# Kernel tuning notes

Measured on AMD Instinct MI355X. Metric: run time of the kernel, lower is better.

Reference implementation:

```python
import jax, jax.numpy as jnp
import numpy as np

N_NODES = 100000
N_EDGES = 1600000
HID = 128
HEADS = 8
DK = HID // HEADS
N_LAYERS = 4
IN_DIM = 32
N_CLASSES = 16


def _ln(x, g, b, eps=1e-5):
    mu = x.mean(-1, keepdims=True)
    var = x.var(-1, keepdims=True)
    return (x - mu) / jnp.sqrt(var + eps) * g + b


def setup_inputs() -> dict:
    key = jax.random.key(0)
    ks = jax.random.split(key, 24)
    s = 0.05
    inp = {
        'feat': jax.random.randint(ks[0], (N_NODES,), 0, IN_DIM, dtype=jnp.int32),
        'edge_src': jax.random.randint(ks[1], (N_EDGES,), 0, N_NODES, dtype=jnp.int32),
        'edge_dst': jnp.sort(jax.random.randint(ks[2], (N_EDGES,), 0, N_NODES, dtype=jnp.int32)),
        'emb': jax.random.normal(ks[3], (IN_DIM, HID), jnp.float32) * s,
        'Wq': jax.random.normal(ks[4], (N_LAYERS, HID, HID), jnp.float32) * s,
        'Wk': jax.random.normal(ks[5], (N_LAYERS, HID, HID), jnp.float32) * s,
        'Wv': jax.random.normal(ks[6], (N_LAYERS, HID, HID), jnp.float32) * s,
        'Wo': jax.random.normal(ks[7], (N_LAYERS, HID, HID), jnp.float32) * s,
        'bo': jnp.zeros((N_LAYERS, HID), jnp.float32),
        'ln1_g': jnp.ones((N_LAYERS, HID), jnp.float32),
        'ln1_b': jnp.zeros((N_LAYERS, HID), jnp.float32),
        'W1': jax.random.normal(ks[8], (N_LAYERS, HID, 2 * HID), jnp.float32) * s,
        'b1': jnp.zeros((N_LAYERS, 2 * HID), jnp.float32),
        'W2': jax.random.normal(ks[9], (N_LAYERS, 2 * HID, HID), jnp.float32) * s,
        'b2': jnp.zeros((N_LAYERS, HID), jnp.float32),
        'ln2_g': jnp.ones((N_LAYERS, HID), jnp.float32),
        'ln2_b': jnp.zeros((N_LAYERS, HID), jnp.float32),
        'mW0': jax.random.normal(ks[10], (HID, HID // 2), jnp.float32) * s,
        'mb0': jnp.zeros((HID // 2,), jnp.float32),
        'mW1': jax.random.normal(ks[11], (HID // 2, HID // 4), jnp.float32) * s,
        'mb1': jnp.zeros((HID // 4,), jnp.float32),
        'mW2': jax.random.normal(ks[12], (HID // 4, N_CLASSES), jnp.float32) * s,
        'mb2': jnp.zeros((N_CLASSES,), jnp.float32),
    }
    return inp


def reference(feat, edge_src, edge_dst, emb, Wq, Wk, Wv, Wo, bo, ln1_g, ln1_b,
              W1, b1, W2, b2, ln2_g, ln2_b, mW0, mb0, mW1, mb1, mW2, mb2):
    N = feat.shape[0]
    h = emb[feat]  # [N, HID] embedding gather
    inv_sqrt_dk = jnp.float32(1.0 / np.sqrt(DK))
    for l in range(Wq.shape[0]):
        h_in1 = h
        q = (h @ Wq[l]).reshape(N, HEADS, DK)
        k = (h @ Wk[l]).reshape(N, HEADS, DK)
        v = (h @ Wv[l]).reshape(N, HEADS, DK)
        # per-edge scores: K[src] . Q[dst], scaled, clipped, exponentiated
        sc = jnp.einsum('ehd,ehd->eh', k[edge_src], q[edge_dst]) * inv_sqrt_dk
        sc = jnp.exp(jnp.clip(sc, -5.0, 5.0))  # [E, HEADS]
        wV = jax.ops.segment_sum(sc[:, :, None] * v[edge_src], edge_dst, num_segments=N)
        z = jax.ops.segment_sum(sc, edge_dst, num_segments=N)
        attn = (wV / (z[:, :, None] + 1e-6)).reshape(N, HID)
        h = h_in1 + (attn @ Wo[l] + bo[l])  # residual + O proj
        h = _ln(h, ln1_g[l], ln1_b[l])
        h_in2 = h
        f = jax.nn.relu(h @ W1[l] + b1[l]) @ W2[l] + b2[l]
        h = _ln(h_in2 + f, ln2_g[l], ln2_b[l])
    # MLPReadout: HID -> HID/2 -> HID/4 -> n_classes
    h = jax.nn.relu(h @ mW0 + mb0)
    h = jax.nn.relu(h @ mW1 + mb1)
    return h @ mW2 + mb2
```

## Files before the change

kernel.cpp:

```cpp
#include <hip/hip_runtime.h>
#include <hip/hip_fp16.h>

#define HID 128
#define N_LAYERS 4
#define IN_DIM 32
#define N_CLASSES 16

typedef _Float16 f16x8 __attribute__((ext_vector_type(8)));
typedef float f32x2 __attribute__((ext_vector_type(2)));
typedef __attribute__((ext_vector_type(4))) float f32x4;
typedef unsigned int uint_t;

#if defined(__has_builtin)
#if __has_builtin(__builtin_amdgcn_cvt_pk_f32_fp8)
#define HAVE_CVT_FP8 1
#endif
#if __has_builtin(__builtin_amdgcn_cvt_pk_fp8_f32)
#define HAVE_ENC_FP8 1
#endif
#endif

__device__ __forceinline__ unsigned short f2bf(float f) {
    unsigned int u = __float_as_uint(f);
    return (unsigned short)((u + 0x7FFFu + ((u >> 16) & 1u)) >> 16);
}
__device__ __forceinline__ float2 up16(uint_t u) {
    __half2 h = *(__half2*)&u;
    return __half22float2(h);
}

__device__ __forceinline__ unsigned char f2e4m3(float f) {
    unsigned int u = __float_as_uint(f);
    unsigned char s = (unsigned char)((u >> 24) & 0x80u);
    unsigned int a = u & 0x7FFFFFFFu;
    if (a >= 0x43E00000u) return s | 0x7Eu;
    int exp = (int)(a >> 23) - 127;
    if (exp < -6) {
        int m = (int)rintf(__uint_as_float(a) * 512.f);
        return s | (unsigned char)m;
    }
    unsigned int lsb = (a >> 20) & 1u;
    a += 0x7FFFFu + lsb;
    int e8 = ((int)(a >> 23) - 127) + 7;
    unsigned int m8 = (a >> 20) & 7u;
    return s | (unsigned char)((e8 << 3) | (int)m8);
}
__device__ __forceinline__ float e4m32f(unsigned int b) {
    unsigned int s = (b & 0x80u) << 24;
    unsigned int E = (b >> 3) & 15u, m = b & 7u;
    if (E == 0) {
        float v = (float)m * 0.001953125f;
        return __uint_as_float(__float_as_uint(v) | s);
    }
    return __uint_as_float(s | ((E + 120u) << 23) | (m << 20));
}
__device__ __forceinline__ unsigned char enc8(float v) {
#ifdef HAVE_ENC_FP8
    int r = __builtin_amdgcn_cvt_pk_fp8_f32(v, v, 0, false);
    return (unsigned char)(r & 0xFF);
#else
    return f2e4m3(v);
#endif
}
__device__ __forceinline__ void dec8v(uint_t u, f32x2* o) {
#ifdef HAVE_CVT_FP8
    o[0] = __builtin_amdgcn_cvt_pk_f32_fp8(u, false);
    o[1] = __builtin_amdgcn_cvt_pk_f32_fp8(u, true);
#else
    o[0] = (f32x2){e4m32f(u & 255u), e4m32f((u >> 8) & 255u)};
    o[1] = (f32x2){e4m32f((u >> 16) & 255u), e4m32f(u >> 24)};
#endif
}

__global__ void detect_kernel(const unsigned int* __restrict__ ln1g, int* __restrict__ flag) {
    if (threadIdx.x == 0 && blockIdx.x == 0)
        *flag = (ln1g[0] == 0x3F800000u) ? 0 : 1;
}

#define NSM 11
struct SArgs {
    const void* src[NSM];
    float*      dst[NSM];
    int         cnt[NSM];
};

__global__ void conv_kernel(SArgs args, const int* __restrict__ flag) {
    int p = blockIdx.y;
    int n = args.cnt[p];
    int base = (blockIdx.x * 256 + threadIdx.x) * 4;
    if (base >= n) return;
    float* dst = args.dst[p];
    if (*flag) {
        const unsigned short* s = (const unsigned short*)args.src[p];
        #pragma unroll
        for (int j = 0; j < 4; ++j)
            dst[base + j] = __uint_as_float(((unsigned int)s[base + j]) << 16);
    } else {
        const float* s = (const float*)args.src[p];
        *(float4*)&dst[base] = *(const float4*)&s[base];
    }
}

#define NW 27
struct WArgs {
    const void* src[NW];
    int         soff[NW];
    _Float16*   dst[NW];
    int         K[NW];
    int         M[NW];
};

__global__ void wconv_kernel(WArgs a, const int* __restrict__ flag) {
    int p = blockIdx.y;
    int K = a.K[p], M = a.M[p];
    int idx = blockIdx.x * 256 + threadIdx.x;
    if (idx >= K * M) return;
    int k = idx / M, m = idx % M;
    float v;
    if (*flag)
        v = __uint_as_float(((unsigned int)((const unsigned short*)a.src[p])[a.soff[p] + idx]) << 16);
    else
        v = ((const float*)a.src[p])[a.soff[p] + idx];
    a.dst[p][(size_t)m * K + k] = (_Float16)v;
}

__global__ void csr_kernel(const int* __restrict__ dst, int* __restrict__ row_start,
                           int N, int E) {
    int n = blockIdx.x * 256 + threadIdx.x;
    if (n > N) return;
    int lo = 0, hi = E;
    while (lo < hi) {
        int mid = (lo + hi) >> 1;
        if (dst[mid] < n) lo = mid + 1; else hi = mid;
    }
    row_start[n] = lo;
}

__global__ void embed_kernel(const int* __restrict__ feat, const float* __restrict__ emb,
                             _Float16* __restrict__ h, int N) {
    int idx = blockIdx.x * 256 + threadIdx.x;
    if (idx >= N * 16) return;
    int n  = idx >> 4;
    int c8 = idx & 15;
    int f = feat[n];
    const float* s = &emb[(size_t)f * HID + c8 * 8];
    float4 a = *(const float4*)s;
    float4 b = *(const float4*)(s + 4);
    f16x8 o;
    o[0] = (_Float16)a.x; o[1] = (_Float16)a.y; o[2] = (_Float16)a.z; o[3] = (_Float16)a.w;
    o[4] = (_Float16)b.x; o[5] = (_Float16)b.y; o[6] = (_Float16)b.z; o[7] = (_Float16)b.w;
    *(f16x8*)&h[(size_t)n * HID + c8 * 8] = o;
}

template<int K, int KC, int MC>
__launch_bounds__(256)
__global__ void mfma_gemm_qkv(const _Float16* __restrict__ Ain,
                              const _Float16* __restrict__ Bt,
                              _Float16* __restrict__ q16, unsigned char* __restrict__ kvp8) {
    constexpr int NT  = MC / 16;
    constexpr int SAB = KC * 2 + 16;

    __shared__ __align__(16) char As[64 * SAB];
    __shared__ __align__(16) char Bs[MC * SAB];

    const int t    = threadIdx.x;
    const int w    = t >> 6;
    const int l    = t & 63;
    const int quad = l >> 4;
    const int lc   = l & 15;
    const int row0 = blockIdx.x * 64;
    const int mbase = blockIdx.y * MC;

    f32x4 acc[NT];
    #pragma unroll
    for (int i = 0; i < NT; ++i) acc[i] = (f32x4){0.f, 0.f, 0.f, 0.f};

    {
        constexpr int AU = 64 * KC / 8;
        #pragma unroll
        for (int i = 0; i < (AU + 255) / 256; ++i) {
            int idx = t + i * 256;
            if ((AU % 256 == 0) || idx < AU) {
                int r = idx / (KC / 8), u = idx % (KC / 8);
                *(uint4*)&As[r * SAB + u * 16] =
                    *(const uint4*)(Ain + (size_t)(row0 + r) * K + u * 8);
            }
        }
        constexpr int BU = MC * KC / 8;
        #pragma unroll
        for (int i = 0; i < (BU + 255) / 256; ++i) {
            int idx = t + i * 256;
            if ((BU % 256 == 0) || idx < BU) {
                int m = idx / (KC / 8), u = idx % (KC / 8);
                *(uint4*)&Bs[m * SAB + u * 16] =
                    *(const uint4*)(Bt + (size_t)(mbase + m) * K + u * 8);
            }
        }
        __syncthreads();
        #pragma unroll
        for (int kk = 0; kk < KC / 32; ++kk) {
            f16x8 af = *(const f16x8*)&As[(w * 16 + lc) * SAB + kk * 64 + quad * 16];
            #pragma unroll
            for (int i = 0; i < NT; ++i) {
                f16x8 bf = *(const f16x8*)&Bs[(i * 16 + lc) * SAB + kk * 64 + quad * 16];
                acc[i] = __builtin_amdgcn_mfma_f32_16x16x32_f16(af, bf, acc[i], 0, 0, 0);
            }
        }
    }

    #pragma unroll
    for (int r = 0; r < 4; ++r) {
        int row = row0 + w * 16 + quad * 4 + r;
        #pragma unroll
        for (int i = 0; i < NT; ++i) {
            float v = acc[i][r];
            int gc = mbase + i * 16 + lc;
            if (gc < 128)      q16[(size_t)row * 128 + gc] = (_Float16)v;
            else if (gc < 256) kvp8[(size_t)row * 256 + (gc - 128)] = enc8(v);
            else               kvp8[(size_t)row * 256 + 128 + (gc - 256)] = enc8(v);
        }
    }
}

template<int NEXTM, bool RMODE>
__launch_bounds__(256)
__global__ void layer_tail_fused(const _Float16* __restrict__ t2, _Float16* __restrict__ h,
                                 const _Float16* __restrict__ Wo, const _Float16* __restrict__ W1,
                                 const _Float16* __restrict__ W2,
                                 const _Float16* __restrict__ Wn, const float* __restrict__ bn,
                                 const float* __restrict__ bo,  const float* __restrict__ l1g,
                                 const float* __restrict__ l1b, const float* __restrict__ b1,
                                 const float* __restrict__ b2,  const float* __restrict__ l2g,
                                 const float* __restrict__ l2b,
                                 _Float16* __restrict__ q16, unsigned char* __restrict__ kvp8) {
    constexpr int SAB = 272;
    __shared__ __align__(16) char bufA[64 * SAB];
    __shared__ __align__(16) char bufH[64 * SAB];
    __shared__ __align__(16) char bufB[64 * SAB];

    const int t = threadIdx.x, w = t >> 6, l = t & 63;
    const int quad = l >> 4, lc = l & 15;
    const int row0 = blockIdx.x * 64;
    const int arow = (w * 16 + lc) * SAB;

    _Float16 resv[4][8];
    #pragma unroll
    for (int r = 0; r < 4; ++r) {
        int row = row0 + w * 16 + quad * 4 + r;
        #pragma unroll
        for (int j = 0; j < 8; ++j)
            resv[r][j] = h[(size_t)row * 128 + j * 16 + lc];
    }

    #pragma unroll
    for (int i = 0; i < 4; ++i) {
        int idx = t + i * 256;
        int r = idx >> 4, u = idx & 15;
        *(uint4*)&bufA[r * SAB + u * 16] = *(const uint4*)(t2 + (size_t)(row0 + r) * 128 + u * 8);
    }

    auto stageW = [&](const _Float16* src, int rowStride) {
        __syncthreads();
        #pragma unroll
        for (int i = 0; i < 4; ++i) {
            int idx = t + i * 256;
            int r = idx >> 4, u = idx & 15;
            *(uint4*)&bufB[r * SAB + u * 16] =
                *(const uint4*)(src + (size_t)r * rowStride + u * 8);
        }
        __syncthreads();
    };
    auto mf4 = [&](const char* Ar, f32x4* acc) {
        #pragma unroll
        for (int kk = 0; kk < 4; ++kk) {
            f16x8 af = *(const f16x8*)(Ar + kk * 64 + quad * 16);
            #pragma unroll
            for (int i = 0; i < 4; ++i) {
                f16x8 bf = *(const f16x8*)&bufB[(i * 16 + lc) * SAB + kk * 64 + quad * 16];
                acc[i] = __builtin_amdgcn_mfma_f32_16x16x32_f16(af, bf, acc[i], 0, 0, 0);
            }
        }
    };

    f32x4 acc[8];
    #pragma unroll
    for (int i = 0; i < 8; ++i) acc[i] = (f32x4){0.f, 0.f, 0.f, 0.f};
    #pragma unroll
    for (int c = 0; c < 2; ++c) {
        stageW(Wo + (size_t)c * 64 * 128, 128);
        mf4(bufA + arow, acc + c * 4);
    }

    {
        float gv[8], bv[8], bb[8];
        #pragma unroll
        for (int j = 0; j < 8; ++j) {
            int col = j * 16 + lc;
            gv[j] = l1g[col]; bv[j] = l1b[col]; bb[j] = bo[col];
        }
        #pragma unroll
        for (int r = 0; r < 4; ++r) {
            int lrow = (w * 16 + quad * 4 + r) * SAB;
            float v[8];
            float s = 0.f, ss = 0.f;
            #pragma unroll
            for (int j = 0; j < 8; ++j) {
                v[j] = acc[j][r] + bb[j] + (float)resv[r][j];
                s += v[j]; ss += v[j] * v[j];
            }
            #pragma unroll
            for (int m = 1; m <= 8; m <<= 1) { s += __shfl_xor(s, m); ss += __shfl_xor(ss, m); }
            float mu   = s * (1.f / 128.f);
            float rstd = rsqrtf(ss * (1.f / 128.f) - mu * mu + 1e-5f);
            #pragma unroll
            for (int j = 0; j < 8; ++j) {
                float o = (v[j] - mu) * rstd * gv[j] + bv[j];
                *(_Float16*)&bufH[lrow + (j * 16 + lc) * 2] = (_Float16)o;
            }
        }
    }

    f32x4 acc3[8];
    #pragma unroll
    for (int i = 0; i < 8; ++i) acc3[i] = (f32x4){0.f, 0.f, 0.f, 0.f};
    #pragma unroll
    for (int half = 0; half < 2; ++half) {
        #pragma unroll
        for (int c2 = 0; c2 < 2; ++c2) {
            int c = half * 2 + c2;
            stageW(W1 + (size_t)c * 64 * 128, 128);
            f32x4 a2[4];
            #pragma unroll
            for (int i = 0; i < 4; ++i) a2[i] = (f32x4){0.f, 0.f, 0.f, 0.f};
            mf4(bufH + arow, a2);
            #pragma unroll
            for (int r = 0; r < 4; ++r) {
                int lrow = (w * 16 + quad * 4 + r) * SAB;
                #pragma unroll
                for (int i = 0; i < 4; ++i) {
                    float v = a2[i][r] + b1[c * 64 + i * 16 + lc];
                    v = fmaxf(v, 0.f);
                    *(_Float16*)&bufA[lrow + c2 * 128 + (i * 16 + lc) * 2] = (_Float16)v;
                }
            }
        }
        #pragma unroll
        for (int cc = 0; cc < 2; ++cc) {
            stageW(W2 + (size_t)cc * 64 * 256 + half * 128, 256);
            mf4(bufA + arow, acc3 + cc * 4);
        }
    }

    {
        float gv[8], bv[8], bb[8];
        #pragma unroll
        for (int j = 0; j < 8; ++j) {
            int col = j * 16 + lc;
            gv[j] = l2g[col]; bv[j] = l2b[col]; bb[j] = b2[col];
        }
        #pragma unroll
        for (int r = 0; r < 4; ++r) {
            int row = row0 + w * 16 + quad * 4 + r;
            int lrow = (w * 16 + quad * 4 + r) * SAB;
            float v[8];
            float s = 0.f, ss = 0.f;
            #pragma unroll
            for (int j = 0; j < 8; ++j) {
                float res = (float)*(const _Float16*)&bufH[lrow + (j * 16 + lc) * 2];
                v[j] = acc3[j][r] + bb[j] + res;
                s += v[j]; ss += v[j] * v[j];
            }
            #pragma unroll
            for (int m = 1; m <= 8; m <<= 1) { s += __shfl_xor(s, m); ss += __shfl_xor(ss, m); }
            float mu   = s * (1.f / 128.f);
            float rstd = rsqrtf(ss * (1.f / 128.f) - mu * mu + 1e-5f);
            #pragma unroll
            for (int j = 0; j < 8; ++j) {
                float o = (v[j] - mu) * rstd * gv[j] + bv[j];
                h[(size_t)row * 128 + j * 16 + lc] = (_Float16)o;
                *(_Float16*)&bufA[lrow + (j * 16 + lc) * 2] = (_Float16)o;
            }
        }
    }

    #pragma unroll
    for (int c = 0; c < NEXTM / 64; ++c) {
        stageW(Wn + (size_t)c * 64 * 128, 128);
        f32x4 a4[4];
        #pragma unroll
        for (int i = 0; i < 4; ++i) a4[i] = (f32x4){0.f, 0.f, 0.f, 0.f};
        mf4(bufA + arow, a4);
        #pragma unroll
        for (int r = 0; r < 4; ++r) {
            int row = row0 + w * 16 + quad * 4 + r;
            #pragma unroll
            for (int i = 0; i < 4; ++i) {
                int gc = c * 64 + i * 16 + lc;
                float v = a4[i][r];
                if (RMODE) {
                    v += bn[gc];
                    v = fmaxf(v, 0.f);
                    q16[(size_t)row * 64 + gc] = (_Float16)v;
                } else {
                    if (gc < 128)      q16[(size_t)row * 128 + gc] = (_Float16)v;
                    else if (gc < 256) kvp8[(size_t)row * 256 + (gc - 128)] = enc8(v);
                    else               kvp8[(size_t)row * 256 + 128 + (gc - 256)] = enc8(v);
                }
            }
        }
    }
}

__launch_bounds__(256)
__global__ void readout_tail(const _Float16* __restrict__ r0,
                             const _Float16* __restrict__ w1t, const float* __restrict__ b1_,
                             const _Float16* __restrict__ w2t, const float* __restrict__ b2_,
                             void* __restrict__ outp, const int* __restrict__ flag, int N) {
    constexpr int SA = 144;
    constexpr int SR = 80;
    __shared__ __align__(16) char bufA[64 * SA];
    __shared__ __align__(16) char bufR[64 * SR];

    const int t    = threadIdx.x;
    const int w    = t >> 6;
    const int l    = t & 63;
    const int quad = l >> 4;
    const int lc   = l & 15;
    const int row0 = blockIdx.x * 64;

    #pragma unroll
    for (int i = 0; i < 2; ++i) {
        int idx = t + i * 256;
        int r = idx >> 3, u = idx & 7;
        *(uint4*)&bufA[r * SA + u * 16] = *(const uint4*)(r0 + (size_t)(row0 + r) * 64 + u * 8);
    }
    __syncthreads();

    f32x4 acc[2];
    acc[0] = (f32x4){0.f, 0.f, 0.f, 0.f};
    acc[1] = (f32x4){0.f, 0.f, 0.f, 0.f};
    #pragma unroll
    for (int kk = 0; kk < 2; ++kk) {
        f16x8 af = *(const f16x8*)&bufA[(w * 16 + lc) * SA + kk * 64 + quad * 16];
        #pragma unroll
        for (int i = 0; i < 2; ++i) {
            f16x8 bf = *(const f16x8*)(w1t + (size_t)(i * 16 + lc) * 64 + kk * 32 + quad * 8);
            acc[i] = __builtin_amdgcn_mfma_f32_16x16x32_f16(af, bf, acc[i], 0, 0, 0);
        }
    }
    #pragma unroll
    for (int r = 0; r < 4; ++r) {
        int lrow = (w * 16 + quad * 4 + r) * SR;
        #pragma unroll
        for (int i = 0; i < 2; ++i) {
            float v = acc[i][r] + b1_[i * 16 + lc];
            v = fmaxf(v, 0.f);
            *(_Float16*)&bufR[lrow + (i * 16 + lc) * 2] = (_Float16)v;
        }
    }
    f32x4 a2 = (f32x4){0.f, 0.f, 0.f, 0.f};
    {
        f16x8 af = *(const f16x8*)&bufR[(w * 16 + lc) * SR + quad * 16];
        f16x8 bf = *(const f16x8*)(w2t + (size_t)lc * 32 + quad * 8);
        a2 = __builtin_amdgcn_mfma_f32_16x16x32_f16(af, bf, a2, 0, 0, 0);
    }
    #pragma unroll
    for (int r = 0; r < 4; ++r) {
        int row = row0 + w * 16 + quad * 4 + r;
        if (row < N) {
            float v = a2[r] + b2_[lc];
            size_t o = (size_t)row * 16 + lc;
            if (*flag) ((unsigned short*)outp)[o] = f2bf(v);
            else       ((float*)outp)[o] = v;
        }
    }
}

__global__ void attn_kernel(const _Float16* __restrict__ q16, const uint_t* __restrict__ kvp,
                            const int* __restrict__ esrc, const int* __restrict__ rows,
                            _Float16* __restrict__ out, int N) {
    int node = (blockIdx.x * blockDim.x + threadIdx.x) >> 6;
    if (node >= N) return;
    int l    = threadIdx.x & 63;
    int head = l & 7;
    int eg   = l >> 3;

    f32x2 qh[8];
    {
        const uint4* qp = (const uint4*)(q16 + (size_t)node * HID + head * 16);
        uint4 q0 = qp[0], q1 = qp[1];
        uint_t qs[8] = {q0.x, q0.y, q0.z, q0.w, q1.x, q1.y, q1.z, q1.w};
        #pragma unroll
        for (int i = 0; i < 8; ++i) {
            float2 f = up16(qs[i]);
            qh[i] = (f32x2){f.x * 0.25f, f.y * 0.25f};
        }
    }
    int e0 = rows[node], e1 = rows[node + 1];
    f32x2 wv[8];
    #pragma unroll
    for (int i = 0; i < 8; ++i) wv[i] = (f32x2){0.f, 0.f};
    float z = 0.f;

    for (int eb = e0; eb < e1; eb += 16) {
        int ea = eb + eg, ec = eb + 8 + eg;
        bool oka = ea < e1, okc = ec < e1;
        int sa  = esrc[oka ? ea : e1 - 1];
        int sc_ = esrc[okc ? ec : e1 - 1];
        uint4 ka = *(const uint4*)(kvp + (size_t)sa  * 64 + head * 4);
        uint4 va = *(const uint4*)(kvp + (size_t)sa  * 64 + 32 + head * 4);
        uint4 kc = *(const uint4*)(kvp + (size_t)sc_ * 64 + head * 4);
        uint4 vc = *(const uint4*)(kvp + (size_t)sc_ * 64 + 32 + head * 4);

        f32x2 k2a[8], k2c[8];
        dec8v(ka.x, k2a); dec8v(ka.y, k2a + 2); dec8v(ka.z, k2a + 4); dec8v(ka.w, k2a + 6);
        dec8v(kc.x, k2c); dec8v(kc.y, k2c + 2); dec8v(kc.z, k2c + 4); dec8v(kc.w, k2c + 6);
        f32x2 da2 = (f32x2){0.f, 0.f}, dc2 = (f32x2){0.f, 0.f};
        #pragma unroll
        for (int j = 0; j < 8; ++j) { da2 += qh[j] * k2a[j]; dc2 += qh[j] * k2c[j]; }
        float da = da2.x + da2.y, dc = dc2.x + dc2.y;
        float sa2 = oka ? __expf(fminf(fmaxf(da, -5.f), 5.f)) : 0.f;
        float sc2 = okc ? __expf(fminf(fmaxf(dc, -5.f), 5.f)) : 0.f;

        f32x2 v2a[8], v2c[8];
        dec8v(va.x, v2a); dec8v(va.y, v2a + 2); dec8v(va.z, v2a + 4); dec8v(va.w, v2a + 6);
        dec8v(vc.x, v2c); dec8v(vc.y, v2c + 2); dec8v(vc.z, v2c + 4); dec8v(vc.w, v2c + 6);
        f32x2 pa = (f32x2){sa2, sa2}, pc = (f32x2){sc2, sc2};
        #pragma unroll
        for (int j = 0; j < 8; ++j) { wv[j] += pa * v2a[j]; wv[j] += pc * v2c[j]; }
        z += sa2 + sc2;
    }
    #pragma unroll
    for (int m = 8; m < 64; m <<= 1) {
        z += __shfl_xor(z, m);
        #pragma unroll
        for (int i = 0; i < 8; ++i) {
            wv[i].x += __shfl_xor(wv[i].x, m);
            wv[i].y += __shfl_xor(wv[i].y, m);
        }
    }
    if (eg == 0) {
        float inv = 1.f / (z + 1e-6f);
        f16x8 o0, o1;
        #pragma unroll
        for (int i = 0; i < 4; ++i) {
            o0[2*i]   = (_Float16)(wv[i].x * inv);
            o0[2*i+1] = (_Float16)(wv[i].y * inv);
            o1[2*i]   = (_Float16)(wv[4+i].x * inv);
            o1[2*i+1] = (_Float16)(wv[4+i].y * inv);
        }
        *(f16x8*)&out[(size_t)node * HID + head * 16]     = o0;
        *(f16x8*)&out[(size_t)node * HID + head * 16 + 8] = o1;
    }
}

extern "C" void kernel_launch(void* const* d_in, const int* in_sizes, int n_in,
                              void* d_out, int out_size, void* d_ws, size_t ws_size,
                              hipStream_t stream) {
    const int N  = in_sizes[0];
    const int E  = in_sizes[1];
    const int RB = (N + 63) / 64;
    const size_t NP = (size_t)RB * 64;

    const int* d_feat = (const int*)d_in[0];
    const int* d_esrc = (const int*)d_in[1];
    const int* d_edst = (const int*)d_in[2];

    char* base = (char*)d_ws;
    size_t cur = 0;
    auto alloc = [&](size_t bytes) -> char* {
        cur = (cur + 255) & ~(size_t)255;
        char* p = base + cur;
        cur += bytes;
        return p;
    };
    int* d_flag = (int*)alloc(4);
    int* d_rows = (int*)alloc((size_t)(N + 1) * 4);

    float* p_emb = (float*)alloc(IN_DIM * HID * 4);
    float* p_bo  = (float*)alloc(N_LAYERS * HID * 4);
    float* p_l1g = (float*)alloc(N_LAYERS * HID * 4);
    float* p_l1b = (float*)alloc(N_LAYERS * HID * 4);
    float* p_b1  = (float*)alloc(N_LAYERS * 2 * HID * 4);
    float* p_b2  = (float*)alloc(N_LAYERS * HID * 4);
    float* p_l2g = (float*)alloc(N_LAYERS * HID * 4);
    float* p_l2b = (float*)alloc(N_LAYERS * HID * 4);
    float* p_mb0 = (float*)alloc(64 * 4);
    float* p_mb1 = (float*)alloc(32 * 4);
    float* p_mb2 = (float*)alloc(16 * 4);

    _Float16* wqkv_t = (_Float16*)alloc((size_t)N_LAYERS * 384 * 128 * 2);
    _Float16* wo_t   = (_Float16*)alloc((size_t)N_LAYERS * 128 * 128 * 2);
    _Float16* w1_t   = (_Float16*)alloc((size_t)N_LAYERS * 256 * 128 * 2);
    _Float16* w2_t   = (_Float16*)alloc((size_t)N_LAYERS * 128 * 256 * 2);
    _Float16* mw0_t  = (_Float16*)alloc(64 * 128 * 2);
    _Float16* mw1_t  = (_Float16*)alloc(32 * 64 * 2);
    _Float16* mw2_t  = (_Float16*)alloc(16 * 32 * 2);

    _Float16*      buf_h = (_Float16*)alloc(NP * HID * 2);
    _Float16*      q16   = (_Float16*)alloc(NP * HID * 2);
    _Float16*      t2    = (_Float16*)alloc(NP * HID * 2);
    unsigned char* kvp   = (unsigned char*)alloc(NP * 256);

    detect_kernel<<<1, 64, 0, stream>>>((const unsigned int*)d_in[9], d_flag);

    {
        SArgs sa;
        const int sidx[NSM] = {3, 8, 9, 10, 12, 14, 15, 16, 18, 20, 22};
        float*    sdst[NSM] = {p_emb, p_bo, p_l1g, p_l1b, p_b1, p_b2, p_l2g, p_l2b, p_mb0, p_mb1, p_mb2};
        const int scnt[NSM] = {IN_DIM*HID, N_LAYERS*HID, N_LAYERS*HID, N_LAYERS*HID,
                               N_LAYERS*2*HID, N_LAYERS*HID, N_LAYERS*HID, N_LAYERS*HID, 64, 32, 16};
        for (int i = 0; i < NSM; ++i) { sa.src[i] = d_in[sidx[i]]; sa.dst[i] = sdst[i]; sa.cnt[i] = scnt[i]; }
        conv_kernel<<<dim3(4, NSM), 256, 0, stream>>>(sa, d_flag);
    }

    {
        WArgs wa;
        int wi = 0;
        auto addw = [&](int inp, int off, int Kd, int Md, _Float16* dst) {
            wa.src[wi] = d_in[inp]; wa.soff[wi] = off; wa.K[wi] = Kd; wa.M[wi] = Md;
            wa.dst[wi] = dst; ++wi;
        };
        for (int l = 0; l < N_LAYERS; ++l) {
            addw(4,  l * 16384, 128, 128, wqkv_t + (size_t)l * 49152);
            addw(5,  l * 16384, 128, 128, wqkv_t + (size_t)l * 49152 + 16384);
            addw(6,  l * 16384, 128, 128, wqkv_t + (size_t)l * 49152 + 32768);
            addw(7,  l * 16384, 128, 128, wo_t + (size_t)l * 16384);
            addw(11, l * 32768, 128, 256, w1_t + (size_t)l * 32768);
            addw(13, l * 32768, 256, 128, w2_t + (size_t)l * 32768);
        }
        addw(17, 0, 128, 64, mw0_t);
        addw(19, 0, 64,  32, mw1_t);
        addw(21, 0, 32,  16, mw2_t);
        wconv_kernel<<<dim3(128, NW), 256, 0, stream>>>(wa, d_flag);
    }

    csr_kernel<<<(N + 1 + 255) / 256, 256, 0, stream>>>(d_edst, d_rows, N, E);
    embed_kernel<<<((size_t)N * 16 + 255) / 256, 256, 0, stream>>>(d_feat, p_emb, buf_h, N);

    const int GBW = (N + 3) / 4;

    mfma_gemm_qkv<128, 128, 192><<<dim3(RB, 2), 256, 0, stream>>>(buf_h, wqkv_t, q16, kvp);

    for (int l = 0; l < N_LAYERS; ++l) {
        const _Float16* Wo = wo_t + (size_t)l * 16384;
        const _Float16* W1 = w1_t + (size_t)l * 32768;
        const _Float16* W2 = w2_t + (size_t)l * 32768;
        const float* bo  = p_bo  + (size_t)l * HID;
        const float* l1g = p_l1g + (size_t)l * HID;
        const float* l1b = p_l1b + (size_t)l * HID;
        const float* b1  = p_b1  + (size_t)l * 2 * HID;
        const float* b2  = p_b2  + (size_t)l * HID;
        const float* l2g = p_l2g + (size_t)l * HID;
        const float* l2b = p_l2b + (size_t)l * HID;

        attn_kernel<<<GBW, 256, 0, stream>>>(q16, (const uint_t*)kvp, d_esrc, d_rows, t2, N);

        if (l < N_LAYERS - 1) {
            layer_tail_fused<384, false><<<RB, 256, 0, stream>>>(
                t2, buf_h, Wo, W1, W2, wqkv_t + (size_t)(l + 1) * 49152, nullptr,
                bo, l1g, l1b, b1, b2, l2g, l2b, q16, kvp);
        } else {
            layer_tail_fused<64, true><<<RB, 256, 0, stream>>>(
                t2, buf_h, Wo, W1, W2, mw0_t, p_mb0,
                bo, l1g, l1b, b1, b2, l2g, l2b, q16, nullptr);
        }
    }

    readout_tail<<<RB, 256, 0, stream>>>(q16, mw1_t, p_mb1, mw2_t, p_mb2, d_out, d_flag, N);
}
```

Before: 841.0 us.

## Double-buffer weight staging with register prefetch in fused layer tail

```diff
diff --git a/kernel.cpp b/kernel.cpp
--- a/kernel.cpp
+++ b/kernel.cpp
@@ -234,9 +234,10 @@
                                  const float* __restrict__ l2b,
                                  _Float16* __restrict__ q16, unsigned char* __restrict__ kvp8) {
     constexpr int SAB = 272;
+    constexpr int NCH = 20 + NEXTM / 32;
     __shared__ __align__(16) char bufA[64 * SAB];
     __shared__ __align__(16) char bufH[64 * SAB];
-    __shared__ __align__(16) char bufB[64 * SAB];
+    __shared__ __align__(16) char bufB[2 * 32 * SAB];
 
     const int t = threadIdx.x, w = t >> 6, l = t & 63;
     const int quad = l >> 4, lc = l & 15;
@@ -252,162 +253,173 @@
             resv[r][j] = h[(size_t)row * 128 + j * 16 + lc];
     }
 
-    #pragma unroll
-    for (int i = 0; i < 4; ++i) {
-        int idx = t + i * 256;
-        int r = idx >> 4, u = idx & 15;
-        *(uint4*)&bufA[r * SAB + u * 16] = *(const uint4*)(t2 + (size_t)(row0 + r) * 128 + u * 8);
-    }
-
-    auto stageW = [&](const _Float16* src, int rowStride) {
-        __syncthreads();
-        #pragma unroll
-        for (int i = 0; i < 4; ++i) {
-            int idx = t + i * 256;
+    uint4 pre[2];
+    auto issueC = [&](int c) {
+        const _Float16* src; int stride;
+        if (c < 4)       { src = Wo + (size_t)c * 4096;              stride = 128; }
+        else if (c < 8)  { src = W1 + (size_t)(c - 4) * 4096;        stride = 128; }
+        else if (c < 12) { src = W2 + (size_t)(c - 8) * 8192;        stride = 256; }
+        else if (c < 16) { src = W1 + (size_t)(c - 8) * 4096;        stride = 128; }
+        else if (c < 20) { src = W2 + (size_t)(c - 16) * 8192 + 128; stride = 256; }
+        else             { src = Wn + (size_t)(c - 20) * 4096;       stride = 128; }
+        #pragma unroll
+        for (int j = 0; j < 2; ++j) {
+            int idx = t + j * 256;
             int r = idx >> 4, u = idx & 15;
-            *(uint4*)&bufB[r * SAB + u * 16] =
-                *(const uint4*)(src + (size_t)r * rowStride + u * 8);
+            pre[j] = *(const uint4*)(src + (size_t)r * stride + u * 8);
+        }
+    };
+    auto commitC = [&](int c) {
+        int boff = (c & 1) * 32 * SAB;
+        #pragma unroll
+        for (int j = 0; j < 2; ++j) {
+            int idx = t + j * 256;
+            int r = idx >> 4, u = idx & 15;
+            *(uint4*)&bufB[boff + r * SAB + u * 16] = pre[j];
         }
         __syncthreads();
     };
-    auto mf4 = [&](const char* Ar, f32x4* acc) {
+    auto mf2 = [&](const char* Ar, int c, f32x4* a2) {
+        int boff = (c & 1) * 32 * SAB;
         #pragma unroll
         for (int kk = 0; kk < 4; ++kk) {
             f16x8 af = *(const f16x8*)(Ar + kk * 64 + quad * 16);
             #pragma unroll
-            for (int i = 0; i < 4; ++i) {
-                f16x8 bf = *(const f16x8*)&bufB[(i * 16 + lc) * SAB + kk * 64 + quad * 16];
-                acc[i] = __builtin_amdgcn_mfma_f32_16x16x32_f16(af, bf, acc[i], 0, 0, 0);
+            for (int i = 0; i < 2; ++i) {
+                f16x8 bf = *(const f16x8*)&bufB[boff + (i * 16 + lc) * SAB + kk * 64 + quad * 16];
+                a2[i] = __builtin_amdgcn_mfma_f32_16x16x32_f16(af, bf, a2[i], 0, 0, 0);
             }
         }
     };
 
-    f32x4 acc[8];
-    #pragma unroll
-    for (int i = 0; i < 8; ++i) acc[i] = (f32x4){0.f, 0.f, 0.f, 0.f};
-    #pragma unroll
-    for (int c = 0; c < 2; ++c) {
-        stageW(Wo + (size_t)c * 64 * 128, 128);
-        mf4(bufA + arow, acc + c * 4);
-    }
-
-    {
-        float gv[8], bv[8], bb[8];
-        #pragma unroll
-        for (int j = 0; j < 8; ++j) {
-            int col = j * 16 + lc;
-            gv[j] = l1g[col]; bv[j] = l1b[col]; bb[j] = bo[col];
-        }
-        #pragma unroll
-        for (int r = 0; r < 4; ++r) {
-            int lrow = (w * 16 + quad * 4 + r) * SAB;
-            float v[8];
-            float s = 0.f, ss = 0.f;
-            #pragma unroll
-            for (int j = 0; j < 8; ++j) {
-                v[j] = acc[j][r] + bb[j] + (float)resv[r][j];
-                s += v[j]; ss += v[j] * v[j];
-            }
-            #pragma unroll
-            for (int m = 1; m <= 8; m <<= 1) { s += __shfl_xor(s, m); ss += __shfl_xor(ss, m); }
-            float mu   = s * (1.f / 128.f);
-            float rstd = rsqrtf(ss * (1.f / 128.f) - mu * mu + 1e-5f);
-            #pragma unroll
-            for (int j = 0; j < 8; ++j) {
-                float o = (v[j] - mu) * rstd * gv[j] + bv[j];
-                *(_Float16*)&bufH[lrow + (j * 16 + lc) * 2] = (_Float16)o;
-            }
-        }
-    }
-
-    f32x4 acc3[8];
-    #pragma unroll
-    for (int i = 0; i < 8; ++i) acc3[i] = (f32x4){0.f, 0.f, 0.f, 0.f};
-    #pragma unroll
-    for (int half = 0; half < 2; ++half) {
-        #pragma unroll
-        for (int c2 = 0; c2 < 2; ++c2) {
-            int c = half * 2 + c2;
-            stageW(W1 + (size_t)c * 64 * 128, 128);
-            f32x4 a2[4];
-            #pragma unroll
-            for (int i = 0; i < 4; ++i) a2[i] = (f32x4){0.f, 0.f, 0.f, 0.f};
-            mf4(bufH + arow, a2);
+    issueC(0);
+    #pragma unroll
+    for (int i = 0; i < 4; ++i) {
+        int idx = i * 64 + l;
+        int rr = idx >> 4, u = idx & 15;
+        *(uint4*)&bufA[(w * 16 + rr) * SAB + u * 16] =
+            *(const uint4*)(t2 + (size_t)(row0 + w * 16 + rr) * 128 + u * 8);
+    }
+    commitC(0);
+
+    f32x4 accO[8], acc3[8];
+    #pragma unroll
+    for (int i = 0; i < 8; ++i) {
+        accO[i] = (f32x4){0.f, 0.f, 0.f, 0.f};
+        acc3[i] = (f32x4){0.f, 0.f, 0.f, 0.f};
+    }
+
+    #pragma unroll
+    for (int c = 0; c < NCH; ++c) {
+        if (c + 1 < NCH) issueC(c + 1);
+
+        if (c < 4) {
+            mf2(bufA + arow, c, accO + 2 * c);
+            if (c == 3) {
+                float gv[8], bv[8], bb[8];
+                #pragma unroll
+                for (int j = 0; j < 8; ++j) {
+                    int col = j * 16 + lc;
+                    gv[j] = l1g[col]; bv[j] = l1b[col]; bb[j] = bo[col];
+                }
+                #pragma unroll
+                for (int r = 0; r < 4; ++r) {
+                    int lrow = (w * 16 + quad * 4 + r) * SAB;
+                    float v[8];
+                    float s = 0.f, ss = 0.f;
+                    #pragma unroll
+                    for (int j = 0; j < 8; ++j) {
+                        v[j] = accO[j][r] + bb[j] + (float)resv[r][j];
+                        s += v[j]; ss += v[j] * v[j];
+                    }
+                    #pragma unroll
+                    for (int m = 1; m <= 8; m <<= 1) { s += __shfl_xor(s, m); ss += __shfl_xor(ss, m); }
+                    float mu   = s * (1.f / 128.f);
+                    float rstd = rsqrtf(ss * (1.f / 128.f) - mu * mu + 1e-5f);
+                    #pragma unroll
+                    for (int j = 0; j < 8; ++j) {
+                        float o = (v[j] - mu) * rstd * gv[j] + bv[j];
+                        *(_Float16*)&bufH[lrow + (j * 16 + lc) * 2] = (_Float16)o;
+                    }
+                }
+            }
+        } else if (c < 8 || (c >= 12 && c < 16)) {
+            const int localj = (c < 8) ? (c - 4) : (c - 12);
+            const int colbase = (c < 8) ? (c - 4) * 32 : 128 + (c - 12) * 32;
+            f32x4 a2[2];
+            a2[0] = (f32x4){0.f, 0.f, 0.f, 0.f};
+            a2[1] = (f32x4){0.f, 0.f, 0.f, 0.f};
+            mf2(bufH + arow, c, a2);
             #pragma unroll
             for (int r = 0; r < 4; ++r) {
                 int lrow = (w * 16 + quad * 4 + r) * SAB;
                 #pragma unroll
-                for (int i = 0; i < 4; ++i) {
-                    float v = a2[i][r] + b1[c * 64 + i * 16 + lc];
+                for (int i = 0; i < 2; ++i) {
+                    float v = a2[i][r] + b1[colbase + i * 16 + lc];
                     v = fmaxf(v, 0.f);
-                    *(_Float16*)&bufA[lrow + c2 * 128 + (i * 16 + lc) * 2] = (_Float16)v;
+                    *(_Float16*)&bufA[lrow + (localj * 32 + i * 16 + lc) * 2] = (_Float16)v;
                 }
             }
-        }
-        #pragma unroll
-        for (int cc = 0; cc < 2; ++cc) {
-            stageW(W2 + (size_t)cc * 64 * 256 + half * 128, 256);
-            mf4(bufA + arow, acc3 + cc * 4);
-        }
-    }
-
-    {
-        float gv[8], bv[8], bb[8];
-        #pragma unroll
-        for (int j = 0; j < 8; ++j) {
-            int col = j * 16 + lc;
-            gv[j] = l2g[col]; bv[j] = l2b[col]; bb[j] = b2[col];
-        }
-        #pragma unroll
-        for (int r = 0; r < 4; ++r) {
-            int row = row0 + w * 16 + quad * 4 + r;
-            int lrow = (w * 16 + quad * 4 + r) * SAB;
-            float v[8];
-            float s = 0.f, ss = 0.f;
+        } else if (c < 12 || (c >= 16 && c < 20)) {
+            const int j2 = (c < 12) ? (c - 8) : (c - 16);
+            mf2(bufA + arow, c, acc3 + 2 * j2);
+            if (c == 19) {
+                float gv[8], bv[8], bb[8];
+                #pragma unroll
+                for (int j = 0; j < 8; ++j) {
+                    int col = j * 16 + lc;
+                    gv[j] = l2g[col]; bv[j] = l2b[col]; bb[j] = b2[col];
+                }
+                #pragma unroll
+                for (int r = 0; r < 4; ++r) {
+                    int row = row0 + w * 16 + quad * 4 + r;
+                    int lrow = (w * 16 + quad * 4 + r) * SAB;
+                    float v[8];
+                    float s = 0.f, ss = 0.f;
+                    #pragma unroll
+                    for (int j = 0; j < 8; ++j) {
+                        float res = (float)*(const _Float16*)&bufH[lrow + (j * 16 + lc) * 2];
+                        v[j] = acc3[j][r] + bb[j] + res;
+                        s += v[j]; ss += v[j] * v[j];
+                    }
+                    #pragma unroll
+                    for (int m = 1; m <= 8; m <<= 1) { s += __shfl_xor(s, m); ss += __shfl_xor(ss, m); }
+                    float mu   = s * (1.f / 128.f);
+                    float rstd = rsqrtf(ss * (1.f / 128.f) - mu * mu + 1e-5f);
+                    #pragma unroll
+                    for (int j = 0; j < 8; ++j) {
+                        float o = (v[j] - mu) * rstd * gv[j] + bv[j];
+                        h[(size_t)row * 128 + j * 16 + lc] = (_Float16)o;
+                        *(_Float16*)&bufA[lrow + (j * 16 + lc) * 2] = (_Float16)o;
+                    }
+                }
+            }
+        } else {
+            f32x4 a4[2];
+            a4[0] = (f32x4){0.f, 0.f, 0.f, 0.f};
+            a4[1] = (f32x4){0.f, 0.f, 0.f, 0.f};
+            mf2(bufA + arow, c, a4);
             #pragma unroll
-            for (int j = 0; j < 8; ++j) {
-                float res = (float)*(const _Float16*)&bufH[lrow + (j * 16 + lc) * 2];
-                v[j] = acc3[j][r] + bb[j] + res;
-                s += v[j]; ss += v[j] * v[j];
-            }
-            #pragma unroll
-            for (int m = 1; m <= 8; m <<= 1) { s += __shfl_xor(s, m); ss += __shfl_xor(ss, m); }
-            float mu   = s * (1.f / 128.f);
-            float rstd = rsqrtf(ss * (1.f / 128.f) - mu * mu + 1e-5f);
-            #pragma unroll
-            for (int j = 0; j < 8; ++j) {
-                float o = (v[j] - mu) * rstd * gv[j] + bv[j];
-                h[(size_t)row * 128 + j * 16 + lc] = (_Float16)o;
-                *(_Float16*)&bufA[lrow + (j * 16 + lc) * 2] = (_Float16)o;
-            }
-        }
-    }
-
-    #pragma unroll
-    for (int c = 0; c < NEXTM / 64; ++c) {
-        stageW(Wn + (size_t)c * 64 * 128, 128);
-        f32x4 a4[4];
-        #pragma unroll
-        for (int i = 0; i < 4; ++i) a4[i] = (f32x4){0.f, 0.f, 0.f, 0.f};
-        mf4(bufA + arow, a4);
-        #pragma unroll
-        for (int r = 0; r < 4; ++r) {
-            int row = row0 + w * 16 + quad * 4 + r;
-            #pragma unroll
-            for (int i = 0; i < 4; ++i) {
-                int gc = c * 64 + i * 16 + lc;
-                float v = a4[i][r];
-                if (RMODE) {
-                    v += bn[gc];
-                    v = fmaxf(v, 0.f);
-                    q16[(size_t)row * 64 + gc] = (_Float16)v;
-                } else {
-                    if (gc < 128)      q16[(size_t)row * 128 + gc] = (_Float16)v;
-                    else if (gc < 256) kvp8[(size_t)row * 256 + (gc - 128)] = enc8(v);
-                    else               kvp8[(size_t)row * 256 + 128 + (gc - 256)] = enc8(v);
+            for (int r = 0; r < 4; ++r) {
+                int row = row0 + w * 16 + quad * 4 + r;
+                #pragma unroll
+                for (int i = 0; i < 2; ++i) {
+                    int gc = (c - 20) * 32 + i * 16 + lc;
+                    float v = a4[i][r];
+                    if (RMODE) {
+                        v += bn[gc];
+                        v = fmaxf(v, 0.f);
+                        q16[(size_t)row * 64 + gc] = (_Float16)v;
+                    } else {
+                        if (gc < 128)      q16[(size_t)row * 128 + gc] = (_Float16)v;
+                        else if (gc < 256) kvp8[(size_t)row * 256 + (gc - 128)] = enc8(v);
+                        else               kvp8[(size_t)row * 256 + 128 + (gc - 256)] = enc8(v);
+                    }
                 }
             }
         }
+
+        if (c + 1 < NCH) commitC(c + 1);
     }
 }
 
```

Result: slower. 1.009 ms (+20.0%).

## Double-buffer pre-swizzled weight chunks via async global-to-LDS loads in layer tail

Applied to the files above, without the earlier changes.

```diff
diff --git a/kernel.cpp b/kernel.cpp
--- a/kernel.cpp
+++ b/kernel.cpp
@@ -17,6 +17,9 @@
 #endif
 #if __has_builtin(__builtin_amdgcn_cvt_pk_fp8_f32)
 #define HAVE_ENC_FP8 1
+#endif
+#if __has_builtin(__builtin_amdgcn_global_load_lds)
+#define HAVE_GLL 1
 #endif
 #endif
 
@@ -71,6 +74,14 @@
     o[1] = (f32x2){e4m32f((u >> 16) & 255u), e4m32f(u >> 24)};
 #endif
 }
+
+#ifdef HAVE_GLL
+typedef __attribute__((address_space(1))) const unsigned int as1_uint;
+typedef __attribute__((address_space(3))) unsigned int as3_uint;
+__device__ __forceinline__ void gll16(const void* g, void* l) {
+    __builtin_amdgcn_global_load_lds((as1_uint*)g, (as3_uint*)l, 16, 0, 0);
+}
+#endif
 
 __global__ void detect_kernel(const unsigned int* __restrict__ ln1g, int* __restrict__ flag) {
     if (threadIdx.x == 0 && blockIdx.x == 0)
@@ -122,6 +133,26 @@
     else
         v = ((const float*)a.src[p])[a.soff[p] + idx];
     a.dst[p][(size_t)m * K + k] = (_Float16)v;
+}
+
+__global__ void img_kernel(const _Float16* __restrict__ Wo, const _Float16* __restrict__ W1,
+                           const _Float16* __restrict__ W2, const _Float16* __restrict__ Wn,
+                           int nch, _Float16* __restrict__ img) {
+    int idx = blockIdx.x * 256 + threadIdx.x;
+    if (idx >= nch * 1024) return;
+    int c = idx >> 10;
+    int m = (idx >> 4) & 63;
+    int u = idx & 15;
+    const _Float16* src; int stride;
+    if (c < 2)       { src = Wo + (size_t)c * 64 * 128;             stride = 128; }
+    else if (c < 4)  { src = W1 + (size_t)(c - 2) * 64 * 128;       stride = 128; }
+    else if (c < 6)  { src = W2 + (size_t)(c - 4) * 64 * 256;       stride = 256; }
+    else if (c < 8)  { src = W1 + (size_t)(c - 4) * 64 * 128;       stride = 128; }
+    else if (c < 10) { src = W2 + (size_t)(c - 8) * 64 * 256 + 128; stride = 256; }
+    else             { src = Wn + (size_t)(c - 10) * 64 * 128;      stride = 128; }
+    f16x8 v = *(const f16x8*)(src + (size_t)m * stride + u * 8);
+    int slot = (u + m) & 15;
+    *(f16x8*)(img + (size_t)c * 8192 + m * 128 + slot * 8) = v;
 }
 
 __global__ void csr_kernel(const int* __restrict__ dst, int* __restrict__ row_start,
@@ -225,23 +256,23 @@
 template<int NEXTM, bool RMODE>
 __launch_bounds__(256)
 __global__ void layer_tail_fused(const _Float16* __restrict__ t2, _Float16* __restrict__ h,
-                                 const _Float16* __restrict__ Wo, const _Float16* __restrict__ W1,
-                                 const _Float16* __restrict__ W2,
-                                 const _Float16* __restrict__ Wn, const float* __restrict__ bn,
+                                 const _Float16* __restrict__ img,
                                  const float* __restrict__ bo,  const float* __restrict__ l1g,
                                  const float* __restrict__ l1b, const float* __restrict__ b1,
                                  const float* __restrict__ b2,  const float* __restrict__ l2g,
-                                 const float* __restrict__ l2b,
+                                 const float* __restrict__ l2b, const float* __restrict__ bn,
                                  _Float16* __restrict__ q16, unsigned char* __restrict__ kvp8) {
     constexpr int SAB = 272;
+    constexpr int NCH = 10 + NEXTM / 64;
     __shared__ __align__(16) char bufA[64 * SAB];
     __shared__ __align__(16) char bufH[64 * SAB];
-    __shared__ __align__(16) char bufB[64 * SAB];
+    __shared__ __align__(16) char bufB[2 * 16384];
 
     const int t = threadIdx.x, w = t >> 6, l = t & 63;
     const int quad = l >> 4, lc = l & 15;
     const int row0 = blockIdx.x * 64;
     const int arow = (w * 16 + lc) * SAB;
+    const char* gimg = (const char*)img;
 
     _Float16 resv[4][8];
     #pragma unroll
@@ -252,162 +283,165 @@
             resv[r][j] = h[(size_t)row * 128 + j * 16 + lc];
     }
 
-    #pragma unroll
-    for (int i = 0; i < 4; ++i) {
-        int idx = t + i * 256;
-        int r = idx >> 4, u = idx & 15;
-        *(uint4*)&bufA[r * SAB + u * 16] = *(const uint4*)(t2 + (size_t)(row0 + r) * 128 + u * 8);
-    }
-
-    auto stageW = [&](const _Float16* src, int rowStride) {
-        __syncthreads();
-        #pragma unroll
-        for (int i = 0; i < 4; ++i) {
-            int idx = t + i * 256;
-            int r = idx >> 4, u = idx & 15;
-            *(uint4*)&bufB[r * SAB + u * 16] =
-                *(const uint4*)(src + (size_t)r * rowStride + u * 8);
-        }
-        __syncthreads();
+#ifdef HAVE_GLL
+    auto issueC = [&](int c) {
+        const char* g = gimg + (size_t)c * 16384 + w * 4096;
+        char* lb = bufB + (c & 1) * 16384 + w * 4096;
+        #pragma unroll
+        for (int i = 0; i < 4; ++i)
+            gll16(g + i * 1024 + l * 16, lb + i * 1024);
     };
-    auto mf4 = [&](const char* Ar, f32x4* acc) {
+#else
+    auto issueC = [&](int c) {
+        const uint4* g = (const uint4*)(gimg + (size_t)c * 16384);
+        uint4* lb = (uint4*)(bufB + (c & 1) * 16384);
+        #pragma unroll
+        for (int i = 0; i < 4; ++i) lb[t + i * 256] = g[t + i * 256];
+    };
+#endif
+    auto mf4 = [&](const char* Ar, int c, f32x4* a) {
+        const char* bb = bufB + (c & 1) * 16384;
         #pragma unroll
         for (int kk = 0; kk < 4; ++kk) {
             f16x8 af = *(const f16x8*)(Ar + kk * 64 + quad * 16);
             #pragma unroll
             for (int i = 0; i < 4; ++i) {
-                f16x8 bf = *(const f16x8*)&bufB[(i * 16 + lc) * SAB + kk * 64 + quad * 16];
-                acc[i] = __builtin_amdgcn_mfma_f32_16x16x32_f16(af, bf, acc[i], 0, 0, 0);
+                int m = i * 16 + lc;
+                int slot = ((kk * 4 + quad) + m) & 15;
+                f16x8 bf = *(const f16x8*)(bb + m * 256 + slot * 16);
+                a[i] = __builtin_amdgcn_mfma_f32_16x16x32_f16(af, bf, a[i], 0, 0, 0);
             }
         }
     };
 
-    f32x4 acc[8];
-    #pragma unroll
-    for (int i = 0; i < 8; ++i) acc[i] = (f32x4){0.f, 0.f, 0.f, 0.f};
-    #pragma unroll
-    for (int c = 0; c < 2; ++c) {
-        stageW(Wo + (size_t)c * 64 * 128, 128);
-        mf4(bufA + arow, acc + c * 4);
-    }
-
-    {
-        float gv[8], bv[8], bb[8];
-        #pragma unroll
-        for (int j = 0; j < 8; ++j) {
-            int col = j * 16 + lc;
-            gv[j] = l1g[col]; bv[j] = l1b[col]; bb[j] = bo[col];
-        }
-        #pragma unroll
-        for (int r = 0; r < 4; ++r) {
-            int lrow = (w * 16 + quad * 4 + r) * SAB;
-            float v[8];
-            float s = 0.f, ss = 0.f;
-            #pragma unroll
-            for (int j = 0; j < 8; ++j) {
-                v[j] = acc[j][r] + bb[j] + (float)resv[r][j];
-                s += v[j]; ss += v[j] * v[j];
+    issueC(0);
+    #pragma unroll
+    for (int i = 0; i < 4; ++i) {
+        int idx = i * 64 + l;
+        int rr = idx >> 4, u = idx & 15;
+        *(uint4*)&bufA[(w * 16 + rr) * SAB + u * 16] =
+            *(const uint4*)(t2 + (size_t)(row0 + w * 16 + rr) * 128 + u * 8);
+    }
+    __syncthreads();
+
+    f32x4 accO[8], acc3[8];
+    #pragma unroll
+    for (int i = 0; i < 8; ++i) {
+        accO[i] = (f32x4){0.f, 0.f, 0.f, 0.f};
+        acc3[i] = (f32x4){0.f, 0.f, 0.f, 0.f};
+    }
+
+    #pragma unroll
+    for (int c = 0; c < NCH; ++c) {
+        if (c + 1 < NCH) issueC(c + 1);
+
+        if (c < 2) {
+            mf4(bufA + arow, c, accO + 4 * c);
+            if (c == 1) {
+                float gv[8], bv[8], bb[8];
+                #pragma unroll
+                for (int j = 0; j < 8; ++j) {
+                    int col = j * 16 + lc;
+                    gv[j] = l1g[col]; bv[j] = l1b[col]; bb[j] = bo[col];
+                }
+                #pragma unroll
+                for (int r = 0; r < 4; ++r) {
+                    int lrow = (w * 16 + quad * 4 + r) * SAB;
+                    float v[8];
+                    float s = 0.f, ss = 0.f;
+                    #pragma unroll
+                    for (int j = 0; j < 8; ++j) {
+                        v[j] = accO[j][r] + bb[j] + (float)resv[r][j];
+                        s += v[j]; ss += v[j] * v[j];
+                    }
+                    #pragma unroll
+                    for (int m = 1; m <= 8; m <<= 1) { s += __shfl_xor(s, m); ss += __shfl_xor(ss, m); }
+                    float mu   = s * (1.f / 128.f);
+                    float rstd = rsqrtf(ss * (1.f / 128.f) - mu * mu + 1e-5f);
+                    #pragma unroll
+                    for (int j = 0; j < 8; ++j) {
+                        float o = (v[j] - mu) * rstd * gv[j] + bv[j];
+                        *(_Float16*)&bufH[lrow + (j * 16 + lc) * 2] = (_Float16)o;
+                    }
+                }
             }
-            #pragma unroll
-            for (int m = 1; m <= 8; m <<= 1) { s += __shfl_xor(s, m); ss += __shfl_xor(ss, m); }
-            float mu   = s * (1.f / 128.f);
-            float rstd = rsqrtf(ss * (1.f / 128.f) - mu * mu + 1e-5f);
-            #pragma unroll
-            for (int j = 0; j < 8; ++j) {
-                float o = (v[j] - mu) * rstd * gv[j] + bv[j];
-                *(_Float16*)&bufH[lrow + (j * 16 + lc) * 2] = (_Float16)o;
-            }
-        }
-    }
-
-    f32x4 acc3[8];
-    #pragma unroll
-    for (int i = 0; i < 8; ++i) acc3[i] = (f32x4){0.f, 0.f, 0.f, 0.f};
-    #pragma unroll
-    for (int half = 0; half < 2; ++half) {
-        #pragma unroll
-        for (int c2 = 0; c2 < 2; ++c2) {
-            int c = half * 2 + c2;
-            stageW(W1 + (size_t)c * 64 * 128, 128);
+        } else if (c == 2 || c == 3 || c == 6 || c == 7) {
+            const int c2 = (c < 4) ? c - 2 : c - 6;
+            const int colbase = (c < 4) ? (c - 2) * 64 : 128 + (c - 6) * 64;
             f32x4 a2[4];
             #pragma unroll
             for (int i = 0; i < 4; ++i) a2[i] = (f32x4){0.f, 0.f, 0.f, 0.f};
-            mf4(bufH + arow, a2);
+            mf4(bufH + arow, c, a2);
             #pragma unroll
             for (int r = 0; r < 4; ++r) {
                 int lrow = (w * 16 + quad * 4 + r) * SAB;
                 #pragma unroll
                 for (int i = 0; i < 4; ++i) {
-                    float v = a2[i][r] + b1[c * 64 + i * 16 + lc];
+                    float v = a2[i][r] + b1[colbase + i * 16 + lc];
                     v = fmaxf(v, 0.f);
                     *(_Float16*)&bufA[lrow + c2 * 128 + (i * 16 + lc) * 2] = (_Float16)v;
                 }
             }
-        }
-        #pragma unroll
-        for (int cc = 0; cc < 2; ++cc) {
-            stageW(W2 + (size_t)cc * 64 * 256 + half * 128, 256);
-            mf4(bufA + arow, acc3 + cc * 4);
-        }
-    }
-
-    {
-        float gv[8], bv[8], bb[8];
-        #pragma unroll
-        for (int j = 0; j < 8; ++j) {
-            int col = j * 16 + lc;
-            gv[j] = l2g[col]; bv[j] = l2b[col]; bb[j] = b2[col];
-        }
-        #pragma unroll
-        for (int r = 0; r < 4; ++r) {
-            int row = row0 + w * 16 + quad * 4 + r;
-            int lrow = (w * 16 + quad * 4 + r) * SAB;
-            float v[8];
-            float s = 0.f, ss = 0.f;
-            #pragma unroll
-            for (int j = 0; j < 8; ++j) {
-                float res = (float)*(const _Float16*)&bufH[lrow + (j * 16 + lc) * 2];
-                v[j] = acc3[j][r] + bb[j] + res;
-                s += v[j]; ss += v[j] * v[j];
-            }
-            #pragma unroll
-            for (int m = 1; m <= 8; m <<= 1) { s += __shfl_xor(s, m); ss += __shfl_xor(ss, m); }
-            float mu   = s * (1.f / 128.f);
-            float rstd = rsqrtf(ss * (1.f / 128.f) - mu * mu + 1e-5f);
-            #pragma unroll
-            for (int j = 0; j < 8; ++j) {
-                float o = (v[j] - mu) * rstd * gv[j] + bv[j];
-                h[(size_t)row * 128 + j * 16 + lc] = (_Float16)o;
-                *(_Float16*)&bufA[lrow + (j * 16 + lc) * 2] = (_Float16)o;
-            }
-        }
-    }
-
-    #pragma unroll
-    for (int c = 0; c < NEXTM / 64; ++c) {
-        stageW(Wn + (size_t)c * 64 * 128, 128);
-        f32x4 a4[4];
-        #pragma unroll
-        for (int i = 0; i < 4; ++i) a4[i] = (f32x4){0.f, 0.f, 0.f, 0.f};
-        mf4(bufA + arow, a4);
-        #pragma unroll
-        for (int r = 0; r < 4; ++r) {
-            int row = row0 + w * 16 + quad * 4 + r;
-            #pragma unroll
-            for (int i = 0; i < 4; ++i) {
-                int gc = c * 64 + i * 16 + lc;
-                float v = a4[i][r];
-                if (RMODE) {
-                    v += bn[gc];
-                    v = fmaxf(v, 0.f);
-                    q16[(size_t)row * 64 + gc] = (_Float16)v;
-                } else {
-                    if (gc < 128)      q16[(size_t)row * 128 + gc] = (_Float16)v;
-                    else if (gc < 256) kvp8[(size_t)row * 256 + (gc - 128)] = enc8(v);
-                    else               kvp8[(size_t)row * 256 + 128 + (gc - 256)] = enc8(v);
+        } else if (c == 4 || c == 5 || c == 8 || c == 9) {
+            const int j2 = (c < 6) ? c - 4 : c - 8;
+            mf4(bufA + arow, c, acc3 + 4 * j2);
+            if (c == 9) {
+                float gv[8], bv[8], bb[8];
+                #pragma unroll
+                for (int j = 0; j < 8; ++j) {
+                    int col = j * 16 + lc;
+                    gv[j] = l2g[col]; bv[j] = l2b[col]; bb[j] = b2[col];
+                }
+                #pragma unroll
+                for (int r = 0; r < 4; ++r) {
+                    int row = row0 + w * 16 + quad * 4 + r;
+                    int lrow = (w * 16 + quad * 4 + r) * SAB;
+                    float v[8];
+                    float s = 0.f, ss = 0.f;
+                    #pragma unroll
+                    for (int j = 0; j < 8; ++j) {
+                        float res = (float)*(const _Float16*)&bufH[lrow + (j * 16 + lc) * 2];
+                        v[j] = acc3[j][r] + bb[j] + res;
+                        s += v[j]; ss += v[j] * v[j];
+                    }
+                    #pragma unroll
+                    for (int m = 1; m <= 8; m <<= 1) { s += __shfl_xor(s, m); ss += __shfl_xor(ss, m); }
+                    float mu   = s * (1.f / 128.f);
+                    float rstd = rsqrtf(ss * (1.f / 128.f) - mu * mu + 1e-5f);
+                    #pragma unroll
+                    for (int j = 0; j < 8; ++j) {
+                        float o = (v[j] - mu) * rstd * gv[j] + bv[j];
+                        h[(size_t)row * 128 + j * 16 + lc] = (_Float16)o;
+                        *(_Float16*)&bufA[lrow + (j * 16 + lc) * 2] = (_Float16)o;
+                    }
                 }
             }
-        }
+        } else {
+            f32x4 a4[4];
+            #pragma unroll
+            for (int i = 0; i < 4; ++i) a4[i] = (f32x4){0.f, 0.f, 0.f, 0.f};
+            mf4(bufA + arow, c, a4);
+            #pragma unroll
+            for (int r = 0; r < 4; ++r) {
+                int row = row0 + w * 16 + quad * 4 + r;
+                #pragma unroll
+                for (int i = 0; i < 4; ++i) {
+                    int gc = (c - 10) * 64 + i * 16 + lc;
+                    float v = a4[i][r];
+                    if (RMODE) {
+                        v += bn[gc];
+                        v = fmaxf(v, 0.f);
+                        q16[(size_t)row * 64 + gc] = (_Float16)v;
+                    } else {
+                        if (gc < 128)      q16[(size_t)row * 128 + gc] = (_Float16)v;
+                        else if (gc < 256) kvp8[(size_t)row * 256 + (gc - 128)] = enc8(v);
+                        else               kvp8[(size_t)row * 256 + 128 + (gc - 256)] = enc8(v);
+                    }
+                }
+            }
+        }
+
+        if (c + 1 < NCH) __syncthreads();
     }
 }
 
@@ -596,6 +630,10 @@
     _Float16* mw0_t  = (_Float16*)alloc(64 * 128 * 2);
     _Float16* mw1_t  = (_Float16*)alloc(32 * 64 * 2);
     _Float16* mw2_t  = (_Float16*)alloc(16 * 32 * 2);
+
+    _Float16* img[N_LAYERS];
+    for (int l = 0; l < N_LAYERS; ++l)
+        img[l] = (_Float16*)alloc(((l < N_LAYERS - 1) ? 16 : 11) * 16384);
 
     _Float16*      buf_h = (_Float16*)alloc(NP * HID * 2);
     _Float16*      q16   = (_Float16*)alloc(NP * HID * 2);
@@ -635,6 +673,15 @@
         wconv_kernel<<<dim3(128, NW), 256, 0, stream>>>(wa, d_flag);
     }
 
+    for (int l = 0; l < N_LAYERS; ++l) {
+        int nch = (l < N_LAYERS - 1) ? 16 : 11;
+        const _Float16* Wn = (l < N_LAYERS - 1) ? wqkv_t + (size_t)(l + 1) * 49152 : mw0_t;
+        img_kernel<<<nch * 4, 256, 0, stream>>>(wo_t + (size_t)l * 16384,
+                                                w1_t + (size_t)l * 32768,
+                                                w2_t + (size_t)l * 32768,
+                                                Wn, nch, img[l]);
+    }
+
     csr_kernel<<<(N + 1 + 255) / 256, 256, 0, stream>>>(d_edst, d_rows, N, E);
     embed_kernel<<<((size_t)N * 16 + 255) / 256, 256, 0, stream>>>(d_feat, p_emb, buf_h, N);
 
@@ -643,9 +690,6 @@
     mfma_gemm_qkv<128, 128, 192><<<dim3(RB, 2), 256, 0, stream>>>(buf_h, wqkv_t, q16, kvp);
 
     for (int l = 0; l < N_LAYERS; ++l) {
-        const _Float16* Wo = wo_t + (size_t)l * 16384;
-        const _Float16* W1 = w1_t + (size_t)l * 32768;
-        const _Float16* W2 = w2_t + (size_t)l * 32768;
         const float* bo  = p_bo  + (size_t)l * HID;
         const float* l1g = p_l1g + (size_t)l * HID;
         const float* l1b = p_l1b + (size_t)l * HID;
@@ -658,12 +702,10 @@
 
         if (l < N_LAYERS - 1) {
             layer_tail_fused<384, false><<<RB, 256, 0, stream>>>(
-                t2, buf_h, Wo, W1, W2, wqkv_t + (size_t)(l + 1) * 49152, nullptr,
-                bo, l1g, l1b, b1, b2, l2g, l2b, q16, kvp);
+                t2, buf_h, img[l], bo, l1g, l1b, b1, b2, l2g, l2b, nullptr, q16, kvp);
         } else {
             layer_tail_fused<64, true><<<RB, 256, 0, stream>>>(
-                t2, buf_h, Wo, W1, W2, mw0_t, p_mb0,
-                bo, l1g, l1b, b1, b2, l2g, l2b, q16, nullptr);
+                t2, buf_h, img[l], bo, l1g, l1b, b1, b2, l2g, l2b, p_mb0, q16, nullptr);
         }
     }
 
```

Measured after the change: 885.9 us. 5.3% more time.
